# Performance work log

Hardware: AMD Instinct MI355X
Metric: run time of the kernel (lower is better)

The kernel has to match this reference:

```python
import jax, jax.numpy as jnp
import numpy as np


def conv3d(x, w, b):
    # x: [B,C,D,H,W], w: [O,I,3,3,3], padding=1, stride=1
    y = jax.lax.conv_general_dilated(
        x, w, window_strides=(1, 1, 1), padding=[(1, 1)] * 3,
        dimension_numbers=("NCDHW", "OIDHW", "NCDHW"))
    return y + b[None, :, None, None, None]


def trilinear_sample(x, cd, ch, cw):
    # x: [B,C,D,H,W]; cd/ch/cw: [B,K,D,H,W] float sampling coords.
    # Zero padding outside the volume (invalid corners masked to 0).
    B, C, D, H, W = x.shape
    d0 = jnp.floor(cd); h0 = jnp.floor(ch); w0 = jnp.floor(cw)
    fd, fh, fw = cd - d0, ch - h0, cw - w0
    d0 = d0.astype(jnp.int32); h0 = h0.astype(jnp.int32); w0 = w0.astype(jnp.int32)
    gather = jax.vmap(lambda xb, z, y, xx: xb[:, z, y, xx])  # -> [B,C,K,D,H,W]
    out = jnp.zeros((B, C) + cd.shape[1:], x.dtype)
    for dz in (0, 1):
        wz = fd if dz else 1.0 - fd
        zi = d0 + dz
        for dy in (0, 1):
            wy = fh if dy else 1.0 - fh
            yi = h0 + dy
            for dx in (0, 1):
                wx = fw if dx else 1.0 - fw
                xi = w0 + dx
                valid = ((zi >= 0) & (zi < D) & (yi >= 0) & (yi < H)
                         & (xi >= 0) & (xi < W)).astype(x.dtype)
                v = gather(x, jnp.clip(zi, 0, D - 1), jnp.clip(yi, 0, H - 1),
                           jnp.clip(xi, 0, W - 1))
                out = out + (wz * wy * wx * valid)[:, None] * v
    return out


def deform_conv3d(x, offsets, mask, w, b):
    # Modulated deformable 3D conv (DCNv2-style), kernel 3x3x3, pad 1, stride 1.
    # offsets: [B,81,D,H,W] = 27 taps x (dd,dh,dw); mask: [B,27,D,H,W].
    B, C, D, H, W = x.shape
    K = 27
    off = offsets.reshape(B, K, 3, D, H, W)
    kd, kh, kw = jnp.meshgrid(jnp.arange(3), jnp.arange(3), jnp.arange(3), indexing="ij")
    tap_d = (kd.reshape(-1) - 1).astype(x.dtype)[None, :, None, None, None]
    tap_h = (kh.reshape(-1) - 1).astype(x.dtype)[None, :, None, None, None]
    tap_w = (kw.reshape(-1) - 1).astype(x.dtype)[None, :, None, None, None]
    gd = jnp.arange(D, dtype=x.dtype)[None, None, :, None, None]
    gh = jnp.arange(H, dtype=x.dtype)[None, None, None, :, None]
    gw = jnp.arange(W, dtype=x.dtype)[None, None, None, None, :]
    cd = gd + tap_d + off[:, :, 0]
    ch = gh + tap_h + off[:, :, 1]
    cw = gw + tap_w + off[:, :, 2]
    sampled = trilinear_sample(x, cd, ch, cw) * mask[:, None]  # [B,C,K,D,H,W]
    out = jnp.einsum("bckdhw,ock->bodhw", sampled, w.reshape(w.shape[0], C, K))
    return out + b[None, :, None, None, None]


def mdconv3d(x, ow, ob, w, b):
    # MDConv3d: internal offset/mask predictor + modulated deformable conv.
    d = conv3d(x, ow, ob)
    offsets, mask = d[:, :81], jax.nn.sigmoid(d[:, 81:])
    return deform_conv3d(x, offsets, mask, w, b)


def forward(x, ow1, ob1, w1, b1, ow2, ob2, w2, b2, ow3, ob3, w3, b3,
            defo_w, defo_b, c3d_w, c3d_b):
    h = jax.nn.relu(mdconv3d(x, ow1, ob1, w1, b1))
    h = jax.nn.relu(mdconv3d(h, ow2, ob2, w2, b2))
    h = jax.nn.relu(mdconv3d(h, ow3, ob3, w3, b3))
    d = conv3d(h, defo_w, defo_b)
    offsets, alpha = d[:, :81], jax.nn.sigmoid(d[:, 81:])
    return deform_conv3d(x, offsets, alpha, c3d_w, c3d_b)


def setup_inputs() -> dict:
    key = jax.random.key(0)
    ks = jax.random.split(key, 16)
    B, C, D, H, W = 1, 256, 8, 32, 32
    M = 256  # mdim
    OFF_SCALE = 0.02  # small init so predicted offsets stay moderate

    def p(k, shape):
        return jax.random.normal(k, shape, jnp.float32) * OFF_SCALE

    inp = {"x": jax.random.normal(ks[0], (B, C, D, H, W), jnp.float32)}
    c_ins = [C, M, M]
    for i, cin in enumerate(c_ins, 1):
        inp[f"ow{i}"] = p(ks[2 * i - 1], (108, cin, 3, 3, 3))
        inp[f"ob{i}"] = jnp.zeros((108,), jnp.float32)
        inp[f"w{i}"] = p(ks[2 * i], (M, cin, 3, 3, 3))
        inp[f"b{i}"] = jnp.zeros((M,), jnp.float32)
    inp["defo_w"] = p(ks[13], (108, M, 3, 3, 3))
    inp["defo_b"] = jnp.zeros((108,), jnp.float32)
    inp["c3d_w"] = p(ks[14], (256, C, 3, 3, 3))
    inp["c3d_b"] = jnp.zeros((256,), jnp.float32)
    return inp


def reference(x, ow1, ob1, w1, b1, ow2, ob2, w2, b2, ow3, ob3, w3, b3,
              defo_w, defo_b, c3d_w, c3d_b):
    return forward(x, ow1, ob1, w1, b1, ow2, ob2, w2, b2, ow3, ob3, w3, b3,
                   defo_w, defo_b, c3d_w, c3d_b)
```

## Files before the change

### kernel.cpp

```cpp
#include <hip/hip_runtime.h>
#include <cstdint>

#define NPOS 8192
#define KTOT 6912
#define XP_ROWS 11560
#define XP_SY 34
#define XP_SZ 1156
#define KS 6
#define KSL 1152

typedef float  facc_t __attribute__((ext_vector_type(4)));
typedef short  bf8_t  __attribute__((ext_vector_type(8)));
typedef unsigned short ub8_t __attribute__((ext_vector_type(8)));

__device__ __forceinline__ unsigned short f2bf(float f) {
    unsigned u = __float_as_uint(f);
    u = (u + 0x7FFFu + ((u >> 16) & 1u)) >> 16;
    return (unsigned short)u;
}
__device__ __forceinline__ float bf2f(unsigned short u) {
    return __uint_as_float(((unsigned)u) << 16);
}

__global__ __launch_bounds__(256) void zero_k(unsigned short* __restrict__ dst) {
    ub8_t zz = {0,0,0,0,0,0,0,0};
    *(ub8_t*)&dst[((size_t)blockIdx.x * 256 + threadIdx.x) * 8] = zz;
}

__global__ __launch_bounds__(256) void pad_x_t(const float* __restrict__ x,
                                               unsigned short* __restrict__ XpA) {
    __shared__ unsigned short T[256 * 33];
    int b = blockIdx.x;
    int z = b >> 5, y = b & 31;
    int t = threadIdx.x;
    int c8 = t >> 5, xv = t & 31;
#pragma unroll 4
    for (int i = 0; i < 32; ++i) {
        int c = i * 8 + c8;
        T[c * 33 + xv] = f2bf(x[c * NPOS + (z << 10) + (y << 5) + xv]);
    }
    __syncthreads();
    int rowb = ((z + 1) * XP_SZ + (y + 1) * XP_SY + 1) * 256;
#pragma unroll 4
    for (int j = 0; j < 32; ++j) {
        XpA[rowb + j * 256 + t] = T[t * 33 + j];
    }
}

__global__ __launch_bounds__(256) void wtrans_all(
    const float* __restrict__ o1, const float* __restrict__ o2,
    const float* __restrict__ o3, const float* __restrict__ o4,
    const float* __restrict__ m1, const float* __restrict__ m2,
    const float* __restrict__ m3, const float* __restrict__ m4,
    unsigned short* __restrict__ wtoff, unsigned short* __restrict__ wtmain) {
    __shared__ float T[6912];
    int b = blockIdx.x, t = threadIdx.x;
    const float* src; unsigned short* dst; int o, O;
    if (b < 512) {
        int L = b >> 7; o = b & 127; O = 108;
        src = (L == 0) ? o1 : (L == 1) ? o2 : (L == 2) ? o3 : o4;
        dst = wtoff + ((size_t)(L * 128 + o)) * KTOT;
    } else {
        int b2 = b - 512;
        int L = b2 >> 8; o = b2 & 255; O = 256;
        src = (L == 0) ? m1 : (L == 1) ? m2 : (L == 2) ? m3 : m4;
        dst = wtmain + ((size_t)(L * 256 + o)) * KTOT;
    }
    if (o < O) {
#pragma unroll 3
        for (int i = 0; i < 27; ++i) T[i * 256 + t] = src[(size_t)o * KTOT + i * 256 + t];
        __syncthreads();
#pragma unroll 3
        for (int i = 0; i < 27; ++i) {
            int kc = i * 256 + t;
            int c = kc & 255, k = kc >> 8;
            dst[kc] = f2bf(T[c * 27 + k]);
        }
    } else {
#pragma unroll 3
        for (int i = 0; i < 27; ++i) dst[i * 256 + t] = 0;
    }
}

template<bool DEFORM>
__global__ __launch_bounds__(256)
void fgemm(const unsigned short* __restrict__ Xp,
           const unsigned short* __restrict__ wt,
           const float* __restrict__ dbuf,
           float* __restrict__ parts) {
    constexpr int O   = DEFORM ? 256 : 128;
    constexpr int PWN = DEFORM ? 4 : 2;
    __shared__ unsigned short Bs[64 * 64] __attribute__((aligned(16)));

    const int t = threadIdx.x;
    const int wave = t >> 6, lane = t & 63;
    const int q = lane >> 4, r = lane & 15;
    const int pbase = blockIdx.x * 64;
    const int ks = blockIdx.y;
    const int kstart = ks * KSL;

    const int obw = DEFORM ? (wave * 64) : ((wave >> 1) * 64);
    const int pfb = DEFORM ? 0 : ((wave & 1) * 32);

    const int pl = t >> 2;
    const int csub = (t & 3) * 16;
    const int p = pbase + pl;
    const int z = p >> 10, y = (p >> 5) & 31, xx = p & 31;
    const int g0 = (t & 3) * 2;
    const int wr0 = pl * 64 + ((g0 ^ (pl & 7)) << 3);
    const int wr1 = pl * 64 + (((g0 + 1) ^ (pl & 7)) << 3);

    facc_t acc[4][PWN];
#pragma unroll
    for (int i = 0; i < 4; ++i)
#pragma unroll
        for (int ip = 0; ip < PWN; ++ip) acc[i][ip] = (facc_t){0.f, 0.f, 0.f, 0.f};

    float cw[8];
    int row0 = 0;
    int kprev = -1;

    for (int chunk = 0; chunk < KSL / 64; ++chunk) {
        const int kc0 = kstart + chunk * 64;
        const int k = kc0 >> 8;
        const int c0 = kc0 & 255;
        const int kd = k / 9, kh = (k / 3) % 3, kw = k % 3;

        bf8_t afr[2][4];
#pragma unroll
        for (int sl = 0; sl < 2; ++sl)
#pragma unroll
            for (int i = 0; i < 4; ++i)
                afr[sl][i] = *(const bf8_t*)&wt[(size_t)(obw + i * 16 + r) * KTOT + kc0 + sl * 32 + q * 8];

        if (DEFORM) {
            if (k != kprev) {
                kprev = k;
                float od  = dbuf[(3 * k + 0) * NPOS + p];
                float oh  = dbuf[(3 * k + 1) * NPOS + p];
                float ow_ = dbuf[(3 * k + 2) * NPOS + p];
                float m   = dbuf[(81 + k) * NPOS + p];
                float cd = (float)(z + kd - 1) + od;
                float ch = (float)(y + kh - 1) + oh;
                float cx = (float)(xx + kw - 1) + ow_;
                float fdf = floorf(cd), fhf = floorf(ch), fwf = floorf(cx);
                float fd = cd - fdf, fh = ch - fhf, fw = cx - fwf;
                float wz0 = 1.f - fd, wz1 = fd;
                float wy0 = 1.f - fh, wy1 = fh;
                float wx0 = 1.f - fw, wx1 = fw;
                int id, ih, iw;
                if (fdf < -1.f || fdf >= 8.f)  { wz0 = 0.f; wz1 = 0.f; id = 0; } else id = (int)fdf;
                if (fhf < -1.f || fhf >= 32.f) { wy0 = 0.f; wy1 = 0.f; ih = 0; } else ih = (int)fhf;
                if (fwf < -1.f || fwf >= 32.f) { wx0 = 0.f; wx1 = 0.f; iw = 0; } else iw = (int)fwf;
                wz0 *= m; wz1 *= m;
                float w00 = wz0 * wy0, w01 = wz0 * wy1, w10 = wz1 * wy0, w11 = wz1 * wy1;
                cw[0] = w00 * wx0; cw[1] = w00 * wx1;
                cw[2] = w01 * wx0; cw[3] = w01 * wx1;
                cw[4] = w10 * wx0; cw[5] = w10 * wx1;
                cw[6] = w11 * wx0; cw[7] = w11 * wx1;
                row0 = (id + 1) * XP_SZ + (ih + 1) * XP_SY + (iw + 1);
            }
            float av[16];
#pragma unroll
            for (int e = 0; e < 16; ++e) av[e] = 0.f;
            const unsigned short* cb = Xp + (size_t)row0 * 256 + c0 + csub;
#pragma unroll
            for (int j = 0; j < 8; ++j) {
                const int roff = ((j >> 2) & 1) * XP_SZ + ((j >> 1) & 1) * XP_SY + (j & 1);
                ub8_t lo = *(const ub8_t*)(cb + roff * 256);
                ub8_t hi = *(const ub8_t*)(cb + roff * 256 + 8);
#pragma unroll
                for (int e = 0; e < 8; ++e) {
                    av[e]     += cw[j] * bf2f(lo[e]);
                    av[8 + e] += cw[j] * bf2f(hi[e]);
                }
            }
            ub8_t v0, v1;
#pragma unroll
            for (int e = 0; e < 8; ++e) { v0[e] = f2bf(av[e]); v1[e] = f2bf(av[8 + e]); }
            *(ub8_t*)&Bs[wr0] = v0;
            *(ub8_t*)&Bs[wr1] = v1;
        } else {
            int row = (z + kd) * XP_SZ + (y + kh) * XP_SY + (xx + kw);
            ub8_t lo = *(const ub8_t*)&Xp[(size_t)row * 256 + c0 + csub];
            ub8_t hi = *(const ub8_t*)&Xp[(size_t)row * 256 + c0 + csub + 8];
            *(ub8_t*)&Bs[wr0] = lo;
            *(ub8_t*)&Bs[wr1] = hi;
        }
        __syncthreads();

#pragma unroll
        for (int sl = 0; sl < 2; ++sl) {
            bf8_t bfr[PWN];
#pragma unroll
            for (int ip = 0; ip < PWN; ++ip) {
                int brow = pfb + ip * 16 + r;
                bfr[ip] = *(const bf8_t*)&Bs[brow * 64 + (((sl * 4 + q) ^ (brow & 7)) << 3)];
            }
#pragma unroll
            for (int i = 0; i < 4; ++i)
#pragma unroll
                for (int ip = 0; ip < PWN; ++ip)
                    acc[i][ip] = __builtin_amdgcn_mfma_f32_16x16x32_bf16(afr[sl][i], bfr[ip], acc[i][ip], 0, 0, 0);
        }
        __syncthreads();
    }

    float* pp = parts + (size_t)ks * O * NPOS;
#pragma unroll
    for (int i = 0; i < 4; ++i)
#pragma unroll
        for (int ip = 0; ip < PWN; ++ip)
#pragma unroll
            for (int reg = 0; reg < 4; ++reg) {
                int o = obw + i * 16 + q * 4 + reg;
                int px = pbase + pfb + ip * 16 + r;
                pp[(size_t)o * NPOS + px] = acc[i][ip][reg];
            }
}

__global__ __launch_bounds__(256) void ccombine(const float* __restrict__ parts,
                                                const float* __restrict__ ob,
                                                float* __restrict__ dbuf) {
    int b = blockIdx.x;
    int o = b >> 3;
    int p4 = ((b & 7) * 256 + threadIdx.x) * 4;
    float s0 = 0, s1 = 0, s2 = 0, s3 = 0;
#pragma unroll
    for (int s = 0; s < KS; ++s) {
        const float4 v = *(const float4*)&parts[((size_t)(s * 128 + o)) * NPOS + p4];
        s0 += v.x; s1 += v.y; s2 += v.z; s3 += v.w;
    }
    float bv = ob[o];
    s0 += bv; s1 += bv; s2 += bv; s3 += bv;
    if (o >= 81) {
        s0 = 1.f / (1.f + __expf(-s0));
        s1 = 1.f / (1.f + __expf(-s1));
        s2 = 1.f / (1.f + __expf(-s2));
        s3 = 1.f / (1.f + __expf(-s3));
    }
    *(float4*)&dbuf[(size_t)o * NPOS + p4] = make_float4(s0, s1, s2, s3);
}

__global__ __launch_bounds__(256) void dcombine_h(const float* __restrict__ parts,
                                                  const float* __restrict__ bias,
                                                  unsigned short* __restrict__ XpB) {
    __shared__ unsigned short T[64 * 66];
    int p0 = blockIdx.x * 64, o0 = blockIdx.y * 64;
    int t = threadIdx.x;
    int pl = t & 63, og = t >> 6;
#pragma unroll 4
    for (int j = 0; j < 16; ++j) {
        int ol = og * 16 + j;
        float s = 0.f;
#pragma unroll
        for (int sp = 0; sp < KS; ++sp)
            s += parts[((size_t)(sp * 256 + o0 + ol)) * NPOS + p0 + pl];
        s += bias[o0 + ol];
        T[ol * 66 + pl] = f2bf(fmaxf(s, 0.f));
    }
    __syncthreads();
    int c = t & 63, pr = t >> 6;
#pragma unroll 4
    for (int j = 0; j < 16; ++j) {
        int pl2 = j * 4 + pr;
        int pg = p0 + pl2;
        int zz = pg >> 10, yy = (pg >> 5) & 31, xv = pg & 31;
        int row = (zz + 1) * XP_SZ + (yy + 1) * XP_SY + xv + 1;
        XpB[(size_t)row * 256 + o0 + c] = T[c * 66 + pl2];
    }
}

__global__ __launch_bounds__(256) void dcombine_out(const float* __restrict__ parts,
                                                    const float* __restrict__ bias,
                                                    float* __restrict__ out) {
    int b = blockIdx.x;
    int o = b >> 3;
    int p4 = ((b & 7) * 256 + threadIdx.x) * 4;
    float s0 = 0, s1 = 0, s2 = 0, s3 = 0;
#pragma unroll
    for (int s = 0; s < KS; ++s) {
        const float4 v = *(const float4*)&parts[((size_t)(s * 256 + o)) * NPOS + p4];
        s0 += v.x; s1 += v.y; s2 += v.z; s3 += v.w;
    }
    float bv = bias[o];
    *(float4*)&out[(size_t)o * NPOS + p4] = make_float4(s0 + bv, s1 + bv, s2 + bv, s3 + bv);
}

extern "C" void kernel_launch(void* const* d_in, const int* in_sizes, int n_in,
                              void* d_out, int out_size, void* d_ws, size_t ws_size,
                              hipStream_t stream) {
    const float* x      = (const float*)d_in[0];
    const float* ow1    = (const float*)d_in[1];
    const float* ob1    = (const float*)d_in[2];
    const float* w1     = (const float*)d_in[3];
    const float* b1     = (const float*)d_in[4];
    const float* ow2    = (const float*)d_in[5];
    const float* ob2    = (const float*)d_in[6];
    const float* w2     = (const float*)d_in[7];
    const float* b2     = (const float*)d_in[8];
    const float* ow3    = (const float*)d_in[9];
    const float* ob3    = (const float*)d_in[10];
    const float* w3     = (const float*)d_in[11];
    const float* b3     = (const float*)d_in[12];
    const float* defo_w = (const float*)d_in[13];
    const float* defo_b = (const float*)d_in[14];
    const float* c3d_w  = (const float*)d_in[15];
    const float* c3d_b  = (const float*)d_in[16];
    float* out = (float*)d_out;

    unsigned short* XpA    = (unsigned short*)d_ws;
    unsigned short* XpB    = XpA + (size_t)XP_ROWS * 256;
    unsigned short* wtoff  = XpB + (size_t)XP_ROWS * 256;
    unsigned short* wtmain = wtoff + (size_t)4 * 128 * KTOT;
    float* dbufp = (float*)(wtmain + (size_t)4 * 256 * KTOT);
    float* parts = dbufp + (size_t)108 * NPOS;

    const dim3 blk(256);
    const dim3 gG(128, KS);

    zero_k<<<2890, blk, 0, stream>>>(XpA);
    pad_x_t<<<256, blk, 0, stream>>>(x, XpA);
    wtrans_all<<<1536, blk, 0, stream>>>(ow1, ow2, ow3, defo_w, w1, w2, w3, c3d_w, wtoff, wtmain);

    const float* cbias[4] = {ob1, ob2, ob3, defo_b};
    const float* dbias[4] = {b1, b2, b3, c3d_b};

    for (int L = 0; L < 4; ++L) {
        const unsigned short* featConv = (L == 0) ? XpA : XpB;
        const unsigned short* featDef  = (L == 3) ? XpA : featConv;
        fgemm<false><<<gG, blk, 0, stream>>>(featConv, wtoff + (size_t)L * 128 * KTOT, nullptr, parts);
        ccombine<<<864, blk, 0, stream>>>(parts, cbias[L], dbufp);
        fgemm<true><<<gG, blk, 0, stream>>>(featDef, wtmain + (size_t)L * 256 * KTOT, dbufp, parts);
        if (L < 3) dcombine_h<<<dim3(128, 4), blk, 0, stream>>>(parts, dbias[L], XpB);
        else       dcombine_out<<<2048, blk, 0, stream>>>(parts, dbias[L], out);
    }
}
```

Baseline: 865.5 us.

## Stage deformable gather through LDS via async global-to-LDS loads with per-tap tables

The deformable GEMM now precomputes per-pixel row indices and trilinear weights once per tap into shared tables. The eight corner rows are fetched with global_load_lds directly into a shared buffer, and the interpolation then reads from LDS. The K chunk shrinks from 64 to 32, the K split grows from 6 to 8 with occupancy hinted at 4 blocks per CU, and weight fragments are loaded inside the MFMA loop. The aim is more coalesced, asynchronous gathers and more parallelism, at the cost of extra barriers per chunk, more LDS use and smaller per-sync work.

```diff
diff --git a/kernel.cpp b/kernel.cpp
--- a/kernel.cpp
+++ b/kernel.cpp
@@ -6,12 +6,13 @@
 #define XP_ROWS 11560
 #define XP_SY 34
 #define XP_SZ 1156
-#define KS 6
-#define KSL 1152
+#define KS 8
+#define KSL 864
 
 typedef float  facc_t __attribute__((ext_vector_type(4)));
 typedef short  bf8_t  __attribute__((ext_vector_type(8)));
 typedef unsigned short ub8_t __attribute__((ext_vector_type(8)));
+typedef float  f4_t   __attribute__((ext_vector_type(4)));
 
 __device__ __forceinline__ unsigned short f2bf(float f) {
     unsigned u = __float_as_uint(f);
@@ -20,6 +21,12 @@
 }
 __device__ __forceinline__ float bf2f(unsigned short u) {
     return __uint_as_float(((unsigned)u) << 16);
+}
+
+__device__ __forceinline__ void gl_lds16(const unsigned short* g, unsigned short* l) {
+    __builtin_amdgcn_global_load_lds(
+        (const __attribute__((address_space(1))) unsigned int*)g,
+        (__attribute__((address_space(3))) unsigned int*)l, 16, 0, 0);
 }
 
 __global__ __launch_bounds__(256) void zero_k(unsigned short* __restrict__ dst) {
@@ -83,14 +90,18 @@
 }
 
 template<bool DEFORM>
-__global__ __launch_bounds__(256)
+__global__ __launch_bounds__(256, 4)
 void fgemm(const unsigned short* __restrict__ Xp,
            const unsigned short* __restrict__ wt,
            const float* __restrict__ dbuf,
            float* __restrict__ parts) {
     constexpr int O   = DEFORM ? 256 : 128;
     constexpr int PWN = DEFORM ? 4 : 2;
-    __shared__ unsigned short Bs[64 * 64] __attribute__((aligned(16)));
+    constexpr int NCH = KSL / 32;
+    __shared__ unsigned short Cbuf[DEFORM ? 16384 : 1] __attribute__((aligned(16)));
+    __shared__ unsigned short Bs[64 * 32] __attribute__((aligned(16)));
+    __shared__ int   rowtab_s[DEFORM ? 64 : 1];
+    __shared__ float cwtab_s[DEFORM ? 512 : 1];
 
     const int t = threadIdx.x;
     const int wave = t >> 6, lane = t & 63;
@@ -103,12 +114,15 @@
     const int pfb = DEFORM ? 0 : ((wave & 1) * 32);
 
     const int pl = t >> 2;
-    const int csub = (t & 3) * 16;
+    const int cg = t & 3;
     const int p = pbase + pl;
     const int z = p >> 10, y = (p >> 5) & 31, xx = p & 31;
-    const int g0 = (t & 3) * 2;
-    const int wr0 = pl * 64 + ((g0 ^ (pl & 7)) << 3);
-    const int wr1 = pl * 64 + (((g0 + 1) ^ (pl & 7)) << 3);
+    const int bswr = pl * 32 + ((cg ^ (pl & 3)) << 3);
+
+    const int sj   = (t >> 2) & 7;
+    const int squad = t & 3;
+    const int sroff = ((sj >> 2) & 1) * XP_SZ + ((sj >> 1) & 1) * XP_SY + (sj & 1);
+    const int sphi = t >> 5;
 
     facc_t acc[4][PWN];
 #pragma unroll
@@ -116,92 +130,86 @@
 #pragma unroll
         for (int ip = 0; ip < PWN; ++ip) acc[i][ip] = (facc_t){0.f, 0.f, 0.f, 0.f};
 
-    float cw[8];
-    int row0 = 0;
-    int kprev = -1;
-
-    for (int chunk = 0; chunk < KSL / 64; ++chunk) {
-        const int kc0 = kstart + chunk * 64;
+    for (int chunk = 0; chunk < NCH; ++chunk) {
+        const int kc0 = kstart + chunk * 32;
         const int k = kc0 >> 8;
         const int c0 = kc0 & 255;
-        const int kd = k / 9, kh = (k / 3) % 3, kw = k % 3;
-
-        bf8_t afr[2][4];
-#pragma unroll
-        for (int sl = 0; sl < 2; ++sl)
-#pragma unroll
-            for (int i = 0; i < 4; ++i)
-                afr[sl][i] = *(const bf8_t*)&wt[(size_t)(obw + i * 16 + r) * KTOT + kc0 + sl * 32 + q * 8];
 
         if (DEFORM) {
-            if (k != kprev) {
-                kprev = k;
-                float od  = dbuf[(3 * k + 0) * NPOS + p];
-                float oh  = dbuf[(3 * k + 1) * NPOS + p];
-                float ow_ = dbuf[(3 * k + 2) * NPOS + p];
-                float m   = dbuf[(81 + k) * NPOS + p];
-                float cd = (float)(z + kd - 1) + od;
-                float ch = (float)(y + kh - 1) + oh;
-                float cx = (float)(xx + kw - 1) + ow_;
-                float fdf = floorf(cd), fhf = floorf(ch), fwf = floorf(cx);
-                float fd = cd - fdf, fh = ch - fhf, fw = cx - fwf;
-                float wz0 = 1.f - fd, wz1 = fd;
-                float wy0 = 1.f - fh, wy1 = fh;
-                float wx0 = 1.f - fw, wx1 = fw;
-                int id, ih, iw;
-                if (fdf < -1.f || fdf >= 8.f)  { wz0 = 0.f; wz1 = 0.f; id = 0; } else id = (int)fdf;
-                if (fhf < -1.f || fhf >= 32.f) { wy0 = 0.f; wy1 = 0.f; ih = 0; } else ih = (int)fhf;
-                if (fwf < -1.f || fwf >= 32.f) { wx0 = 0.f; wx1 = 0.f; iw = 0; } else iw = (int)fwf;
-                wz0 *= m; wz1 *= m;
-                float w00 = wz0 * wy0, w01 = wz0 * wy1, w10 = wz1 * wy0, w11 = wz1 * wy1;
-                cw[0] = w00 * wx0; cw[1] = w00 * wx1;
-                cw[2] = w01 * wx0; cw[3] = w01 * wx1;
-                cw[4] = w10 * wx0; cw[5] = w10 * wx1;
-                cw[6] = w11 * wx0; cw[7] = w11 * wx1;
-                row0 = (id + 1) * XP_SZ + (ih + 1) * XP_SY + (iw + 1);
-            }
-            float av[16];
-#pragma unroll
-            for (int e = 0; e < 16; ++e) av[e] = 0.f;
-            const unsigned short* cb = Xp + (size_t)row0 * 256 + c0 + csub;
-#pragma unroll
-            for (int j = 0; j < 8; ++j) {
-                const int roff = ((j >> 2) & 1) * XP_SZ + ((j >> 1) & 1) * XP_SY + (j & 1);
-                ub8_t lo = *(const ub8_t*)(cb + roff * 256);
-                ub8_t hi = *(const ub8_t*)(cb + roff * 256 + 8);
-#pragma unroll
-                for (int e = 0; e < 8; ++e) {
-                    av[e]     += cw[j] * bf2f(lo[e]);
-                    av[8 + e] += cw[j] * bf2f(hi[e]);
+            if (chunk == 0 || c0 == 0) {
+                if (t < 64) {
+                    const int kd = k / 9, kh = (k / 3) % 3, kw = k % 3;
+                    int pp = pbase + t;
+                    int zz2 = pp >> 10, yy2 = (pp >> 5) & 31, xx2 = pp & 31;
+                    float od  = dbuf[(3 * k + 0) * NPOS + pp];
+                    float oh  = dbuf[(3 * k + 1) * NPOS + pp];
+                    float ow_ = dbuf[(3 * k + 2) * NPOS + pp];
+                    float m   = dbuf[(81 + k) * NPOS + pp];
+                    float cd = (float)(zz2 + kd - 1) + od;
+                    float ch = (float)(yy2 + kh - 1) + oh;
+                    float cx = (float)(xx2 + kw - 1) + ow_;
+                    float fdf = floorf(cd), fhf = floorf(ch), fwf = floorf(cx);
+                    float fd = cd - fdf, fh = ch - fhf, fw = cx - fwf;
+                    float wz0 = 1.f - fd, wz1 = fd;
+                    float wy0 = 1.f - fh, wy1 = fh;
+                    float wx0 = 1.f - fw, wx1 = fw;
+                    int id, ih, iw;
+                    if (fdf < -1.f || fdf >= 8.f)  { wz0 = 0.f; wz1 = 0.f; id = 0; } else id = (int)fdf;
+                    if (fhf < -1.f || fhf >= 32.f) { wy0 = 0.f; wy1 = 0.f; ih = 0; } else ih = (int)fhf;
+                    if (fwf < -1.f || fwf >= 32.f) { wx0 = 0.f; wx1 = 0.f; iw = 0; } else iw = (int)fwf;
+                    wz0 *= m; wz1 *= m;
+                    float w00 = wz0 * wy0, w01 = wz0 * wy1, w10 = wz1 * wy0, w11 = wz1 * wy1;
+                    rowtab_s[t] = (id + 1) * XP_SZ + (ih + 1) * XP_SY + (iw + 1);
+                    cwtab_s[t * 8 + 0] = w00 * wx0; cwtab_s[t * 8 + 1] = w00 * wx1;
+                    cwtab_s[t * 8 + 2] = w01 * wx0; cwtab_s[t * 8 + 3] = w01 * wx1;
+                    cwtab_s[t * 8 + 4] = w10 * wx0; cwtab_s[t * 8 + 5] = w10 * wx1;
+                    cwtab_s[t * 8 + 6] = w11 * wx0; cwtab_s[t * 8 + 7] = w11 * wx1;
                 }
-            }
-            ub8_t v0, v1;
-#pragma unroll
-            for (int e = 0; e < 8; ++e) { v0[e] = f2bf(av[e]); v1[e] = f2bf(av[8 + e]); }
-            *(ub8_t*)&Bs[wr0] = v0;
-            *(ub8_t*)&Bs[wr1] = v1;
+                __syncthreads();
+            }
+#pragma unroll
+            for (int i = 0; i < 8; ++i) {
+                int plo = i * 8 + sphi;
+                int row = rowtab_s[plo] + sroff;
+                gl_lds16(Xp + (size_t)row * 256 + c0 + squad * 8,
+                         &Cbuf[(i * 256 + (t & ~63)) * 8]);
+            }
+            __syncthreads();
+            {
+                f4_t cw0 = *(const f4_t*)&cwtab_s[pl * 8];
+                f4_t cw1 = *(const f4_t*)&cwtab_s[pl * 8 + 4];
+                float av[8];
+#pragma unroll
+                for (int e = 0; e < 8; ++e) av[e] = 0.f;
+#pragma unroll
+                for (int j = 0; j < 8; ++j) {
+                    ub8_t v = *(const ub8_t*)&Cbuf[pl * 256 + j * 32 + cg * 8];
+                    float w = (j < 4) ? cw0[j] : cw1[j - 4];
+#pragma unroll
+                    for (int e = 0; e < 8; ++e) av[e] += w * bf2f(v[e]);
+                }
+                ub8_t pk;
+#pragma unroll
+                for (int e = 0; e < 8; ++e) pk[e] = f2bf(av[e]);
+                *(ub8_t*)&Bs[bswr] = pk;
+            }
         } else {
+            const int kd = k / 9, kh = (k / 3) % 3, kw = k % 3;
             int row = (z + kd) * XP_SZ + (y + kh) * XP_SY + (xx + kw);
-            ub8_t lo = *(const ub8_t*)&Xp[(size_t)row * 256 + c0 + csub];
-            ub8_t hi = *(const ub8_t*)&Xp[(size_t)row * 256 + c0 + csub + 8];
-            *(ub8_t*)&Bs[wr0] = lo;
-            *(ub8_t*)&Bs[wr1] = hi;
+            ub8_t v = *(const ub8_t*)&Xp[(size_t)row * 256 + c0 + cg * 8];
+            *(ub8_t*)&Bs[bswr] = v;
         }
         __syncthreads();
 
 #pragma unroll
-        for (int sl = 0; sl < 2; ++sl) {
-            bf8_t bfr[PWN];
+        for (int i = 0; i < 4; ++i) {
+            bf8_t a = *(const bf8_t*)&wt[(size_t)(obw + i * 16 + r) * KTOT + kc0 + q * 8];
 #pragma unroll
             for (int ip = 0; ip < PWN; ++ip) {
                 int brow = pfb + ip * 16 + r;
-                bfr[ip] = *(const bf8_t*)&Bs[brow * 64 + (((sl * 4 + q) ^ (brow & 7)) << 3)];
-            }
-#pragma unroll
-            for (int i = 0; i < 4; ++i)
-#pragma unroll
-                for (int ip = 0; ip < PWN; ++ip)
-                    acc[i][ip] = __builtin_amdgcn_mfma_f32_16x16x32_bf16(afr[sl][i], bfr[ip], acc[i][ip], 0, 0, 0);
+                bf8_t b = *(const bf8_t*)&Bs[brow * 32 + ((q ^ (brow & 3)) << 3)];
+                acc[i][ip] = __builtin_amdgcn_mfma_f32_16x16x32_bf16(a, b, acc[i][ip], 0, 0, 0);
+            }
         }
         __syncthreads();
     }
```

New measurement: 862.1 us. Within noise of the previous version (-0.4%).
